# Kernel tuning notes

Hardware: AMD Instinct MI355X
Metric: run time of the kernel (lower is better)

The kernel has to match this reference:

```python
import jax, jax.numpy as jnp
import numpy as np
from jax import lax

BS, SL, T = 1024, 512, 64


def setup_inputs() -> dict:
    key = jax.random.key(0)
    k_e, k_tags, k_st, k_et, k_t = jax.random.split(key, 5)
    e = jax.random.normal(k_e, (BS, SL, T), dtype=jnp.float32)
    tags = jax.random.randint(k_tags, (BS, SL), 0, T, dtype=jnp.int32)
    mask = jnp.ones((BS, SL), dtype=bool)
    st = jax.random.uniform(k_st, (T,), minval=-0.1, maxval=0.1, dtype=jnp.float32)
    et = jax.random.uniform(k_et, (T,), minval=-0.1, maxval=0.1, dtype=jnp.float32)
    t = jax.random.uniform(k_t, (T, T), minval=-0.1, maxval=0.1, dtype=jnp.float32)
    return {"e": e, "tags": tags, "mask": mask, "st": st, "et": et, "t": t}


def reference(e, tags, mask, st, et, t):
    # time-major: [sl, bs, T], [sl, bs], [sl, bs]
    e_t = jnp.transpose(e, (1, 0, 2))
    tags_t = tags.T
    mask_t = mask.T
    sl, bs = tags_t.shape
    idx = jnp.arange(bs)

    # gold path score and partition-function init at step 0
    score0 = st[tags_t[0]] + e_t[0, idx, tags_t[0]]          # [bs]
    norm0 = st[None, :] + e_t[0]                              # [bs, T]

    def step(carry, xs):
        score, normalize = carry
        tag_prev, tag_next, e_next, m_next = xs
        mf = m_next.astype(e_next.dtype)
        score = score + (t[tag_prev, tag_next] + e_next[idx, tag_next]) * mf
        # logsumexp over previous tag: [bs, T_prev, T_next] -> [bs, T_next]
        ns = jax.nn.logsumexp(normalize[:, :, None] + t[None, :, :] + e_next[:, None, :], axis=1)
        normalize = jnp.where(m_next[:, None], ns, normalize)
        return (score, normalize), None

    xs = (tags_t[:-1], tags_t[1:], e_t[1:], mask_t[1:])
    (score, normalize), _ = lax.scan(step, (score0, norm0), xs)

    last = mask_t.sum(axis=0) - 1                             # [bs]
    score = score + et[tags_t[last, idx]]
    logZ = jax.nn.logsumexp(normalize + et[None, :], axis=1)  # [bs]
    total = mask.sum().astype(e.dtype)
    return (score - logZ).sum() / total
```

## Files before the change

### kernel.cpp

```cpp
#include <hip/hip_runtime.h>
#include <hip/hip_bf16.h>

#define BS 1024
#define SL 512
#define T  64

typedef float f32x4 __attribute__((ext_vector_type(4)));
typedef short bf16x8 __attribute__((ext_vector_type(8)));
typedef int   i32x4  __attribute__((ext_vector_type(4)));

union FragU { i32x4 i; bf16x8 v; };

__device__ __forceinline__ float wave_reduce_sum(float x) {
#pragma unroll
    for (int m = 32; m >= 1; m >>= 1) x += __shfl_xor(x, m, 64);
    return x;
}

__device__ __forceinline__ int pk2(float a, float b) {
    union { __hip_bfloat162 h; int i; } u;
    u.h = __float22bfloat162_rn(make_float2(a, b));
    return u.i;
}

__device__ __forceinline__ float dpp_xor1(float x) {
    return __int_as_float(__builtin_amdgcn_update_dpp(
        0, __float_as_int(x), 0xB1, 0xF, 0xF, true));
}

#define MFMA16(A_, B_, C_) __builtin_amdgcn_mfma_f32_16x16x32_bf16((A_), (B_), (C_), 0, 0, 0)

#define BBUILD(BF_, C_, NT_)                                                  \
    {                                                                         \
        const int kb_ = q8 + 32 * (C_), nn_ = nbase + 16 * (NT_);             \
        FragU u_;                                                             \
        u_.i.x = pk2(__expf(t[(kb_ + 0) * T + nn_]), __expf(t[(kb_ + 1) * T + nn_])); \
        u_.i.y = pk2(__expf(t[(kb_ + 2) * T + nn_]), __expf(t[(kb_ + 3) * T + nn_])); \
        u_.i.z = pk2(__expf(t[(kb_ + 4) * T + nn_]), __expf(t[(kb_ + 5) * T + nn_])); \
        u_.i.w = pk2(__expf(t[(kb_ + 6) * T + nn_]), __expf(t[(kb_ + 7) * T + nn_])); \
        BF_ = u_.v;                                                           \
    }

#define STEP(EA_, EB_, APPLY_)                                                \
    {                                                                         \
        float geA_ = __expf(EA_);                                             \
        float geB_ = __expf(EB_);                                             \
        if (APPLY_) { geA_ *= pscale; geB_ *= pscale; }                       \
        f32x4 c0 = zf, c1 = zf, c2 = zf, c3 = zf;                             \
        c0 = MFMA16(A0, B00, c0); c1 = MFMA16(A0, B01, c1);                   \
        c2 = MFMA16(A0, B02, c2); c3 = MFMA16(A0, B03, c3);                   \
        c0 = MFMA16(A1, B10, c0); c1 = MFMA16(A1, B11, c1);                   \
        c2 = MFMA16(A1, B12, c2); c3 = MFMA16(A1, B13, c3);                   \
        const float sA_ = (g & 2) ? c1.x : c0.x;    \
        const float sB_ = (g & 2) ? c3.x : c2.x;    \
        sAc = sA_ * geA_;                                                     \
        sBc = sB_ * geB_;                                                     \
        const int pA_ = pk2(sAc, dpp_xor1(sAc));                              \
        const int pB_ = pk2(sBc, dpp_xor1(sBc));                              \
        FragU uA_, uB_;                                                       \
        uA_.i.x = __builtin_amdgcn_ds_bpermute(ad0, pA_);                     \
        uA_.i.y = __builtin_amdgcn_ds_bpermute(ad1, pA_);                     \
        uA_.i.z = __builtin_amdgcn_ds_bpermute(ad2, pA_);                     \
        uA_.i.w = __builtin_amdgcn_ds_bpermute(ad3, pA_);                     \
        uB_.i.x = __builtin_amdgcn_ds_bpermute(ad0, pB_);                     \
        uB_.i.y = __builtin_amdgcn_ds_bpermute(ad1, pB_);                     \
        uB_.i.z = __builtin_amdgcn_ds_bpermute(ad2, pB_);                     \
        uB_.i.w = __builtin_amdgcn_ds_bpermute(ad3, pB_);                     \
        A0 = uA_.v; A1 = uB_.v;                                               \
    }

#define RESCALE()                                                             \
    {                                                                         \
        const int mb_ = __builtin_amdgcn_readfirstlane(__float_as_int(sAc));  \
        const int ex_ = ((mb_ >> 23) & 0xff) - 126;                           \
        pscale = __int_as_float((127 - ex_) << 23);                           \
        logscale += (float)ex_ * 0.6931471805599453f;                         \
    }

__global__ __launch_bounds__(64, 1) __attribute__((amdgpu_waves_per_eu(1, 1)))
void crf_fused_kernel(const float* __restrict__ e,
                      const float* __restrict__ st, const float* __restrict__ et,
                      const float* __restrict__ t, float* __restrict__ ws) {
    const int b = blockIdx.x;
    const int L = threadIdx.x;
    const int c = L & 15;
    const int g = L >> 4;
    const int q8 = g * 8;
    const int nbase = c;
    const float* ebase = e + (size_t)b * (SL * T);

    const int nA = c + 16 * (g >> 1);
    const float* ebA = ebase + nA;
    const float* ebB = ebase + nA + 32;

    const int adH = (g >> 1) << 7;
    const int ad0 = (((8 * g + 0) & 15) << 2) + adH;
    const int ad1 = (((8 * g + 2) & 15) << 2) + adH;
    const int ad2 = (((8 * g + 4) & 15) << 2) + adH;
    const int ad3 = (((8 * g + 6) & 15) << 2) + adH;

    const f32x4 zf = {0.f, 0.f, 0.f, 0.f};

    bf16x8 B00, B01, B02, B03, B10, B11, B12, B13;
    BBUILD(B00, 0, 0) BBUILD(B01, 0, 1) BBUILD(B02, 0, 2) BBUILD(B03, 0, 3)
    BBUILD(B10, 1, 0) BBUILD(B11, 1, 1) BBUILD(B12, 1, 2) BBUILD(B13, 1, 3)

    bf16x8 A0, A1;
    {
        const f32x4 ea0 = *(const f32x4*)(ebase + 8 * g);
        const f32x4 ea1 = *(const f32x4*)(ebase + 8 * g + 4);
        const f32x4 eb0 = *(const f32x4*)(ebase + 32 + 8 * g);
        const f32x4 eb1 = *(const f32x4*)(ebase + 32 + 8 * g + 4);
        const f32x4 s0 = *(const f32x4*)(st + 8 * g);
        const f32x4 s1 = *(const f32x4*)(st + 8 * g + 4);
        const f32x4 s2 = *(const f32x4*)(st + 32 + 8 * g);
        const f32x4 s3 = *(const f32x4*)(st + 32 + 8 * g + 4);
        FragU u0, u1;
        u0.i.x = pk2(__expf(ea0.x + s0.x), __expf(ea0.y + s0.y));
        u0.i.y = pk2(__expf(ea0.z + s0.z), __expf(ea0.w + s0.w));
        u0.i.z = pk2(__expf(ea1.x + s1.x), __expf(ea1.y + s1.y));
        u0.i.w = pk2(__expf(ea1.z + s1.z), __expf(ea1.w + s1.w));
        u1.i.x = pk2(__expf(eb0.x + s2.x), __expf(eb0.y + s2.y));
        u1.i.y = pk2(__expf(eb0.z + s2.z), __expf(eb0.w + s2.w));
        u1.i.z = pk2(__expf(eb1.x + s3.x), __expf(eb1.y + s3.y));
        u1.i.w = pk2(__expf(eb1.z + s3.z), __expf(eb1.w + s3.w));
        A0 = u0.v; A1 = u1.v;
    }

    const float etA = et[nA];
    const float etB = et[nA + 32];

    float logscale = 0.0f;
    float pscale = 1.0f;
    float sAc = 0.0f, sBc = 0.0f;

    float rA0 = ebA[1 * T], rA1 = ebA[2 * T], rA2 = ebA[3 * T], rA3 = ebA[4 * T];
    float rA4 = ebA[5 * T], rA5 = ebA[6 * T], rA6 = ebA[7 * T], rA7 = ebA[8 * T];
    float rA8 = ebA[9 * T], rA9 = ebA[10 * T], rA10 = ebA[11 * T], rA11 = ebA[12 * T];
    float rB0 = ebB[1 * T], rB1 = ebB[2 * T], rB2 = ebB[3 * T], rB3 = ebB[4 * T];
    float rB4 = ebB[5 * T], rB5 = ebB[6 * T], rB6 = ebB[7 * T], rB7 = ebB[8 * T];
    float rB8 = ebB[9 * T], rB9 = ebB[10 * T], rB10 = ebB[11 * T], rB11 = ebB[12 * T];

    for (int base = 1; base <= SL - 4; base += 4) {
        const int p0 = min(base + 12, SL - 1), p1 = min(base + 13, SL - 1);
        const int p2 = min(base + 14, SL - 1), p3 = min(base + 15, SL - 1);
        const float nA0 = ebA[(size_t)p0 * T], nA1 = ebA[(size_t)p1 * T];
        const float nA2 = ebA[(size_t)p2 * T], nA3 = ebA[(size_t)p3 * T];
        const float nB0 = ebB[(size_t)p0 * T], nB1 = ebB[(size_t)p1 * T];
        const float nB2 = ebB[(size_t)p2 * T], nB3 = ebB[(size_t)p3 * T];

        STEP(rA0, rB0, 1)
        STEP(rA1, rB1, 0)
        STEP(rA2, rB2, 0)
        STEP(rA3, rB3, 0)
        RESCALE()

        rA0 = rA4;  rA1 = rA5;  rA2 = rA6;  rA3 = rA7;
        rA4 = rA8;  rA5 = rA9;  rA6 = rA10; rA7 = rA11;
        rA8 = nA0;  rA9 = nA1;  rA10 = nA2; rA11 = nA3;
        rB0 = rB4;  rB1 = rB5;  rB2 = rB6;  rB3 = rB7;
        rB4 = rB8;  rB5 = rB9;  rB6 = rB10; rB7 = rB11;
        rB8 = nB0;  rB9 = nB1;  rB10 = nB2; rB11 = nB3;
    }
    STEP(rA0, rB0, 1)
    STEP(rA1, rB1, 0)
    STEP(rA2, rB2, 0)

    float zs = sAc * __expf(etA) + sBc * __expf(etB);
    zs = wave_reduce_sum(zs) * 0.5f;
    if (L == 0) ws[b] = -(__logf(zs) + logscale);
}

__global__ __launch_bounds__(64)
void score_kernel(const float* __restrict__ e, const int* __restrict__ tags,
                  const float* __restrict__ st, const float* __restrict__ et,
                  const float* __restrict__ t, float* __restrict__ ws) {
    const int b = blockIdx.x;
    const int j = threadIdx.x;
    const float* ebase = e + (size_t)b * (SL * T);
    const int* tb = tags + b * SL;
    float scp = 0.0f;
#pragma unroll
    for (int i = 0; i < 8; ++i) {
        const int s = j + (i << 6);
        if (s >= 1) {
            const int tc = tb[s];
            const int tp = tb[s - 1];
            scp += t[(tp << 6) + tc] + ebase[(size_t)s * T + tc];
        }
    }
    if (j == 0) {
        const int t0 = tb[0];
        scp += st[t0] + ebase[t0] + et[tb[SL - 1]];
    }
    scp = wave_reduce_sum(scp);
    if (j == 0) ws[b] = ws[b] + scp;
}

__global__ __launch_bounds__(256)
void final_kernel(const float* __restrict__ ws, float* __restrict__ out) {
    const int tid = threadIdx.x;
    float x = (ws[tid] + ws[tid + 256]) + (ws[tid + 512] + ws[tid + 768]);
    x = wave_reduce_sum(x);
    __shared__ float sm[4];
    if ((tid & 63) == 0) sm[tid >> 6] = x;
    __syncthreads();
    if (tid == 0) out[0] = ((sm[0] + sm[1]) + (sm[2] + sm[3])) / (float)(BS * SL);
}

extern "C" void kernel_launch(void* const* d_in, const int* in_sizes, int n_in,
                              void* d_out, int out_size, void* d_ws, size_t ws_size,
                              hipStream_t stream) {
    const float* e    = (const float*)d_in[0];
    const int*   tags = (const int*)d_in[1];
    const float* st   = (const float*)d_in[3];
    const float* et   = (const float*)d_in[4];
    const float* t    = (const float*)d_in[5];
    float* out = (float*)d_out;
    float* ws  = (float*)d_ws;

    crf_fused_kernel<<<BS, 64, 0, stream>>>(e, st, et, t, ws);
    score_kernel<<<BS, 64, 0, stream>>>(e, tags, st, et, t, ws);
    final_kernel<<<1, 256, 0, stream>>>(ws, out);
}
```

Measured before the change: 260.0 us.

## Split CRF forward recursion into concurrent forward and backward waves per sequence

Each block now runs two waves: one carries the forward alpha recursion from the start and the other a backward beta recursion from the end using the transposed transition matrix, each covering about half the sequence. The two halves are combined through shared memory with a dot product to get the partition function. The gold-path score kernel is folded into the same kernel, which removes one launch and a second pass over e. This roughly halves the serial dependency chain per sequence at the cost of twice the waves per block, a transposed strided load of t, and an LDS combine step.

```diff
diff --git a/kernel.cpp b/kernel.cpp
--- a/kernel.cpp
+++ b/kernel.cpp
@@ -34,10 +34,10 @@
     {                                                                         \
         const int kb_ = q8 + 32 * (C_), nn_ = nbase + 16 * (NT_);             \
         FragU u_;                                                             \
-        u_.i.x = pk2(__expf(t[(kb_ + 0) * T + nn_]), __expf(t[(kb_ + 1) * T + nn_])); \
-        u_.i.y = pk2(__expf(t[(kb_ + 2) * T + nn_]), __expf(t[(kb_ + 3) * T + nn_])); \
-        u_.i.z = pk2(__expf(t[(kb_ + 4) * T + nn_]), __expf(t[(kb_ + 5) * T + nn_])); \
-        u_.i.w = pk2(__expf(t[(kb_ + 6) * T + nn_]), __expf(t[(kb_ + 7) * T + nn_])); \
+        u_.i.x = pk2(__expf(t[(kb_ + 0) * sK + nn_ * sN]), __expf(t[(kb_ + 1) * sK + nn_ * sN])); \
+        u_.i.y = pk2(__expf(t[(kb_ + 2) * sK + nn_ * sN]), __expf(t[(kb_ + 3) * sK + nn_ * sN])); \
+        u_.i.z = pk2(__expf(t[(kb_ + 4) * sK + nn_ * sN]), __expf(t[(kb_ + 5) * sK + nn_ * sN])); \
+        u_.i.w = pk2(__expf(t[(kb_ + 6) * sK + nn_ * sN]), __expf(t[(kb_ + 7) * sK + nn_ * sN])); \
         BF_ = u_.v;                                                           \
     }
 
@@ -77,21 +77,35 @@
         logscale += (float)ex_ * 0.6931471805599453f;                         \
     }
 
-__global__ __launch_bounds__(64, 1) __attribute__((amdgpu_waves_per_eu(1, 1)))
-void crf_fused_kernel(const float* __restrict__ e,
+#define EROW(Q_) (ebase + (size_t)(r0row + rdir * (Q_)) * T)
+
+__global__ __launch_bounds__(128, 2)
+void crf_fused_kernel(const float* __restrict__ e, const int* __restrict__ tags,
                       const float* __restrict__ st, const float* __restrict__ et,
                       const float* __restrict__ t, float* __restrict__ ws) {
     const int b = blockIdx.x;
-    const int L = threadIdx.x;
+    const int tid = threadIdx.x;
+    const int w = tid >> 6;
+    const int L = tid & 63;
     const int c = L & 15;
     const int g = L >> 4;
     const int q8 = g * 8;
     const int nbase = c;
     const float* ebase = e + (size_t)b * (SL * T);
+    const int* tb = tags + b * SL;
+
+    const int4 tg = *(const int4*)(tb + 4 * tid);
+    const int tpv = (tid > 0) ? tb[4 * tid - 1] : 0;
+    float scp;
+    if (tid > 0) scp = t[(tpv << 6) + tg.x] + ebase[(size_t)(4 * tid) * T + tg.x];
+    else         scp = st[tg.x] + ebase[tg.x];
+    scp += t[(tg.x << 6) + tg.y] + ebase[(size_t)(4 * tid + 1) * T + tg.y];
+    scp += t[(tg.y << 6) + tg.z] + ebase[(size_t)(4 * tid + 2) * T + tg.z];
+    scp += t[(tg.z << 6) + tg.w] + ebase[(size_t)(4 * tid + 3) * T + tg.w];
+    if (tid == 127) scp += et[tg.w];
 
     const int nA = c + 16 * (g >> 1);
-    const float* ebA = ebase + nA;
-    const float* ebB = ebase + nA + 32;
+    const int nB = nA + 32;
 
     const int adH = (g >> 1) << 7;
     const int ad0 = (((8 * g + 0) & 15) << 2) + adH;
@@ -101,20 +115,27 @@
 
     const f32x4 zf = {0.f, 0.f, 0.f, 0.f};
 
+    const int sK = w ? 1 : T;
+    const int sN = w ? T : 1;
+    const int r0row = w ? (SL - 1) : 0;
+    const int rdir = w ? -1 : 1;
+
     bf16x8 B00, B01, B02, B03, B10, B11, B12, B13;
     BBUILD(B00, 0, 0) BBUILD(B01, 0, 1) BBUILD(B02, 0, 2) BBUILD(B03, 0, 3)
     BBUILD(B10, 1, 0) BBUILD(B11, 1, 1) BBUILD(B12, 1, 2) BBUILD(B13, 1, 3)
 
     bf16x8 A0, A1;
     {
-        const f32x4 ea0 = *(const f32x4*)(ebase + 8 * g);
-        const f32x4 ea1 = *(const f32x4*)(ebase + 8 * g + 4);
-        const f32x4 eb0 = *(const f32x4*)(ebase + 32 + 8 * g);
-        const f32x4 eb1 = *(const f32x4*)(ebase + 32 + 8 * g + 4);
-        const f32x4 s0 = *(const f32x4*)(st + 8 * g);
-        const f32x4 s1 = *(const f32x4*)(st + 8 * g + 4);
-        const f32x4 s2 = *(const f32x4*)(st + 32 + 8 * g);
-        const f32x4 s3 = *(const f32x4*)(st + 32 + 8 * g + 4);
+        const float* er0 = ebase + (size_t)r0row * T;
+        const float* bias = w ? et : st;
+        const f32x4 ea0 = *(const f32x4*)(er0 + 8 * g);
+        const f32x4 ea1 = *(const f32x4*)(er0 + 8 * g + 4);
+        const f32x4 eb0 = *(const f32x4*)(er0 + 32 + 8 * g);
+        const f32x4 eb1 = *(const f32x4*)(er0 + 32 + 8 * g + 4);
+        const f32x4 s0 = *(const f32x4*)(bias + 8 * g);
+        const f32x4 s1 = *(const f32x4*)(bias + 8 * g + 4);
+        const f32x4 s2 = *(const f32x4*)(bias + 32 + 8 * g);
+        const f32x4 s3 = *(const f32x4*)(bias + 32 + 8 * g + 4);
         FragU u0, u1;
         u0.i.x = pk2(__expf(ea0.x + s0.x), __expf(ea0.y + s0.y));
         u0.i.y = pk2(__expf(ea0.z + s0.z), __expf(ea0.w + s0.w));
@@ -127,27 +148,23 @@
         A0 = u0.v; A1 = u1.v;
     }
 
-    const float etA = et[nA];
-    const float etB = et[nA + 32];
-
     float logscale = 0.0f;
     float pscale = 1.0f;
     float sAc = 0.0f, sBc = 0.0f;
 
-    float rA0 = ebA[1 * T], rA1 = ebA[2 * T], rA2 = ebA[3 * T], rA3 = ebA[4 * T];
-    float rA4 = ebA[5 * T], rA5 = ebA[6 * T], rA6 = ebA[7 * T], rA7 = ebA[8 * T];
-    float rA8 = ebA[9 * T], rA9 = ebA[10 * T], rA10 = ebA[11 * T], rA11 = ebA[12 * T];
-    float rB0 = ebB[1 * T], rB1 = ebB[2 * T], rB2 = ebB[3 * T], rB3 = ebB[4 * T];
-    float rB4 = ebB[5 * T], rB5 = ebB[6 * T], rB6 = ebB[7 * T], rB7 = ebB[8 * T];
-    float rB8 = ebB[9 * T], rB9 = ebB[10 * T], rB10 = ebB[11 * T], rB11 = ebB[12 * T];
-
-    for (int base = 1; base <= SL - 4; base += 4) {
-        const int p0 = min(base + 12, SL - 1), p1 = min(base + 13, SL - 1);
-        const int p2 = min(base + 14, SL - 1), p3 = min(base + 15, SL - 1);
-        const float nA0 = ebA[(size_t)p0 * T], nA1 = ebA[(size_t)p1 * T];
-        const float nA2 = ebA[(size_t)p2 * T], nA3 = ebA[(size_t)p3 * T];
-        const float nB0 = ebB[(size_t)p0 * T], nB1 = ebB[(size_t)p1 * T];
-        const float nB2 = ebB[(size_t)p2 * T], nB3 = ebB[(size_t)p3 * T];
+    float rA0 = EROW(1)[nA], rA1 = EROW(2)[nA], rA2 = EROW(3)[nA], rA3 = EROW(4)[nA];
+    float rA4 = EROW(5)[nA], rA5 = EROW(6)[nA], rA6 = EROW(7)[nA], rA7 = EROW(8)[nA];
+    float rA8 = EROW(9)[nA], rA9 = EROW(10)[nA], rA10 = EROW(11)[nA], rA11 = EROW(12)[nA];
+    float rB0 = EROW(1)[nB], rB1 = EROW(2)[nB], rB2 = EROW(3)[nB], rB3 = EROW(4)[nB];
+    float rB4 = EROW(5)[nB], rB5 = EROW(6)[nB], rB6 = EROW(7)[nB], rB7 = EROW(8)[nB];
+    float rB8 = EROW(9)[nB], rB9 = EROW(10)[nB], rB10 = EROW(11)[nB], rB11 = EROW(12)[nB];
+
+    for (int base = 1; base <= 249; base += 4) {
+        const int p0 = base + 12, p1 = base + 13, p2 = base + 14, p3 = base + 15;
+        const float nA0 = EROW(p0)[nA], nA1 = EROW(p1)[nA];
+        const float nA2 = EROW(p2)[nA], nA3 = EROW(p3)[nA];
+        const float nB0 = EROW(p0)[nB], nB1 = EROW(p1)[nB];
+        const float nB2 = EROW(p2)[nB], nB3 = EROW(p3)[nB];
 
         STEP(rA0, rB0, 1)
         STEP(rA1, rB1, 0)
@@ -162,39 +179,30 @@
         rB4 = rB8;  rB5 = rB9;  rB6 = rB10; rB7 = rB11;
         rB8 = nB0;  rB9 = nB1;  rB10 = nB2; rB11 = nB3;
     }
-    STEP(rA0, rB0, 1)
-    STEP(rA1, rB1, 0)
-    STEP(rA2, rB2, 0)
-
-    float zs = sAc * __expf(etA) + sBc * __expf(etB);
-    zs = wave_reduce_sum(zs) * 0.5f;
-    if (L == 0) ws[b] = -(__logf(zs) + logscale);
-}
-
-__global__ __launch_bounds__(64)
-void score_kernel(const float* __restrict__ e, const int* __restrict__ tags,
-                  const float* __restrict__ st, const float* __restrict__ et,
-                  const float* __restrict__ t, float* __restrict__ ws) {
-    const int b = blockIdx.x;
-    const int j = threadIdx.x;
-    const float* ebase = e + (size_t)b * (SL * T);
-    const int* tb = tags + b * SL;
-    float scp = 0.0f;
-#pragma unroll
-    for (int i = 0; i < 8; ++i) {
-        const int s = j + (i << 6);
-        if (s >= 1) {
-            const int tc = tb[s];
-            const int tp = tb[s - 1];
-            scp += t[(tp << 6) + tc] + ebase[(size_t)s * T + tc];
-        }
-    }
-    if (j == 0) {
-        const int t0 = tb[0];
-        scp += st[t0] + ebase[t0] + et[tb[SL - 1]];
-    }
-    scp = wave_reduce_sum(scp);
-    if (j == 0) ws[b] = ws[b] + scp;
+    if (w == 0) {
+        STEP(rA0, rB0, 1)
+        STEP(rA1, rB1, 0)
+        STEP(rA2, rB2, 0)
+        STEP(rA3, rB3, 0)
+    } else {
+        STEP(rA0, rB0, 1)
+        STEP(rA1, rB1, 0)
+        STEP(0.0f, 0.0f, 0)
+    }
+
+    __shared__ float fb2[2][T];
+    __shared__ float lsW[2], scW[2];
+    fb2[w][nA] = sAc;
+    fb2[w][nB] = sBc;
+    const float scs = wave_reduce_sum(scp);
+    if (L == 0) { lsW[w] = logscale; scW[w] = scs; }
+    __syncthreads();
+    if (w == 0) {
+        float zz = fb2[0][L] * fb2[1][L];
+        zz = wave_reduce_sum(zz);
+        if (L == 0)
+            ws[b] = (scW[0] + scW[1]) - (__logf(zz) + lsW[0] + lsW[1]);
+    }
 }
 
 __global__ __launch_bounds__(256)
@@ -219,7 +227,6 @@
     float* out = (float*)d_out;
     float* ws  = (float*)d_ws;
 
-    crf_fused_kernel<<<BS, 64, 0, stream>>>(e, st, et, t, ws);
-    score_kernel<<<BS, 64, 0, stream>>>(e, tags, st, et, t, ws);
+    crf_fused_kernel<<<BS, 128, 0, stream>>>(e, tags, st, et, t, ws);
     final_kernel<<<1, 256, 0, stream>>>(ws, out);
 }
```

New measurement: 268.8 us. 3.4% more time.
